# Optimization experiments

Hardware: AMD Instinct MI355X
Metric: run time of the kernel (lower is better)

The kernel has to match this reference:

```python
import jax, jax.numpy as jnp
import numpy as np

B, T, D = 32, 512, 768
DUR_MAX = 8.0


def length_regulate(x, dur):
    # dur[dur < 0] = 0; reps = (dur + 0.5).long()  (floor of dur+0.5 for dur >= 0)
    dur = jnp.maximum(dur, 0.0)
    reps = jnp.floor(dur + 0.5).astype(jnp.int32)          # [B, T]
    cum = jnp.cumsum(reps, axis=1)                          # [B, T] end offsets
    totals = cum[:, -1]                                     # [B] per-sample lengths
    t_out = int(jnp.max(totals))                            # padded output length (data-dependent, eager)
    pos = jnp.arange(t_out, dtype=jnp.int32)                # [Tout]
    # For output slot j, source token index = searchsorted(cum, j, 'right')
    idx = jax.vmap(lambda c: jnp.searchsorted(c, pos, side='right'))(cum)  # [B, Tout]
    idx = jnp.minimum(idx, x.shape[1] - 1)                  # clamp padding region
    out = jnp.take_along_axis(x, idx[..., None], axis=1)    # [B, Tout, D] gather
    mask = pos[None, :] < totals[:, None]                   # [B, Tout]
    return jnp.where(mask[..., None], out, jnp.zeros((), x.dtype))


def setup_inputs() -> dict:
    key = jax.random.key(0)
    k1, k2 = jax.random.split(key)
    x = jax.random.normal(k1, (B, T, D), dtype=jnp.float32)
    dur = jax.random.uniform(k2, (B, T), dtype=jnp.float32, minval=0.0, maxval=DUR_MAX)
    return {"x": x, "dur": dur}


def reference(x, dur):
    return length_regulate(x, dur)
```

## Files before the change

### kernel.cpp

```cpp
#include <hip/hip_runtime.h>

#define BB 32
#define TT 512
#define DD 768
#define ROWS_PER_BLOCK 8
#define VEC_PER_ROW (DD / 4)

__global__ __launch_bounds__(TT) void lr_scan_kernel(
    const float* __restrict__ dur, int* __restrict__ cum) {
    __shared__ int s[TT];
    const int b = blockIdx.x;
    const int t = threadIdx.x;
    float d = dur[b * TT + t];
    d = fmaxf(d, 0.0f);
    s[t] = (int)floorf(d + 0.5f);
    __syncthreads();
    #pragma unroll
    for (int off = 1; off < TT; off <<= 1) {
        int v = (t >= off) ? s[t - off] : 0;
        __syncthreads();
        s[t] += v;
        __syncthreads();
    }
    cum[b * TT + t] = s[t];
}

__global__ __launch_bounds__(VEC_PER_ROW) void lr_gather_kernel(
    const float* __restrict__ x, const int* __restrict__ cum,
    float* __restrict__ out, int t_out) {
    __shared__ int scum[TT];
    const int b = blockIdx.y;
    const int tid = threadIdx.x;

    for (int i = tid; i < TT; i += VEC_PER_ROW) scum[i] = cum[b * TT + i];
    __syncthreads();

    const int total = scum[TT - 1];
    const int row0 = blockIdx.x * ROWS_PER_BLOCK;

    const float4* xb = (const float4*)(x + (size_t)b * TT * DD);
    float4* ob = (float4*)(out + (size_t)b * (size_t)t_out * DD);

    #pragma unroll
    for (int r = 0; r < ROWS_PER_BLOCK; ++r) {
        const int pos = row0 + r;
        if (pos >= t_out) break;
        float4 v;
        if (pos >= total) {
            v = make_float4(0.f, 0.f, 0.f, 0.f);
        } else {
            int lo = 0, hi = TT;
            while (lo < hi) {
                int mid = (lo + hi) >> 1;
                if (scum[mid] <= pos) lo = mid + 1; else hi = mid;
            }
            int idx = lo < (TT - 1) ? lo : (TT - 1);
            v = xb[(size_t)idx * VEC_PER_ROW + tid];
        }
        ob[(size_t)pos * VEC_PER_ROW + tid] = v;
    }
}

extern "C" void kernel_launch(void* const* d_in, const int* in_sizes, int n_in,
                              void* d_out, int out_size, void* d_ws, size_t ws_size,
                              hipStream_t stream) {
    const float* x   = (const float*)d_in[0];
    const float* dur = (const float*)d_in[1];
    float* out = (float*)d_out;
    int* cum = (int*)d_ws;

    const int t_out = out_size / (BB * DD);

    lr_scan_kernel<<<BB, TT, 0, stream>>>(dur, cum);

    dim3 grid((t_out + ROWS_PER_BLOCK - 1) / ROWS_PER_BLOCK, BB);
    lr_gather_kernel<<<grid, VEC_PER_ROW, 0, stream>>>(x, cum, out, t_out);
}
```

Before: 265.3 us.

## Replace per-row binary-search gather with per-token scatter plus tail zeroing

Switches from a gather, where each output row binary-searches the cumulative durations in shared memory, to a scatter, where each source token is loaded once and written to its contiguous output range. A separate kernel zeroes the padding tail beyond each sample's total length. This removes the per-row search and the repeated reads of the same source row, in exchange for an extra kernel launch and per-block work that now varies with each token's duration.

```diff
diff --git a/kernel.cpp b/kernel.cpp
--- a/kernel.cpp
+++ b/kernel.cpp
@@ -3,8 +3,9 @@
 #define BB 32
 #define TT 512
 #define DD 768
-#define ROWS_PER_BLOCK 8
 #define VEC_PER_ROW (DD / 4)
+#define TOK_PER_BLOCK 8
+#define TAIL_ROWS 8
 
 __global__ __launch_bounds__(TT) void lr_scan_kernel(
     const float* __restrict__ dur, int* __restrict__ cum) {
@@ -25,7 +26,7 @@
     cum[b * TT + t] = s[t];
 }
 
-__global__ __launch_bounds__(VEC_PER_ROW) void lr_gather_kernel(
+__global__ __launch_bounds__(VEC_PER_ROW) void lr_scatter_kernel(
     const float* __restrict__ x, const int* __restrict__ cum,
     float* __restrict__ out, int t_out) {
     __shared__ int scum[TT];
@@ -35,29 +36,38 @@
     for (int i = tid; i < TT; i += VEC_PER_ROW) scum[i] = cum[b * TT + i];
     __syncthreads();
 
-    const int total = scum[TT - 1];
-    const int row0 = blockIdx.x * ROWS_PER_BLOCK;
-
+    const int s0 = blockIdx.x * TOK_PER_BLOCK;
     const float4* xb = (const float4*)(x + (size_t)b * TT * DD);
     float4* ob = (float4*)(out + (size_t)b * (size_t)t_out * DD);
 
     #pragma unroll
-    for (int r = 0; r < ROWS_PER_BLOCK; ++r) {
+    for (int k = 0; k < TOK_PER_BLOCK; ++k) {
+        const int t = s0 + k;
+        const int start = (t == 0) ? 0 : scum[t - 1];
+        const int end = scum[t];
+        if (end > start) {
+            const float4 v = xb[(size_t)t * VEC_PER_ROW + tid];
+            for (int p = start; p < end; ++p)
+                ob[(size_t)p * VEC_PER_ROW + tid] = v;
+        }
+    }
+}
+
+__global__ __launch_bounds__(VEC_PER_ROW) void lr_zero_tail_kernel(
+    const int* __restrict__ cum, float* __restrict__ out, int t_out) {
+    const int b = blockIdx.y;
+    const int total = cum[b * TT + (TT - 1)];
+    const int row0 = blockIdx.x * TAIL_ROWS;
+    if (row0 + TAIL_ROWS <= total) return;
+
+    const int tid = threadIdx.x;
+    float4* ob = (float4*)(out + (size_t)b * (size_t)t_out * DD);
+    const float4 z = make_float4(0.f, 0.f, 0.f, 0.f);
+    #pragma unroll
+    for (int r = 0; r < TAIL_ROWS; ++r) {
         const int pos = row0 + r;
-        if (pos >= t_out) break;
-        float4 v;
-        if (pos >= total) {
-            v = make_float4(0.f, 0.f, 0.f, 0.f);
-        } else {
-            int lo = 0, hi = TT;
-            while (lo < hi) {
-                int mid = (lo + hi) >> 1;
-                if (scum[mid] <= pos) lo = mid + 1; else hi = mid;
-            }
-            int idx = lo < (TT - 1) ? lo : (TT - 1);
-            v = xb[(size_t)idx * VEC_PER_ROW + tid];
-        }
-        ob[(size_t)pos * VEC_PER_ROW + tid] = v;
+        if (pos >= total && pos < t_out)
+            ob[(size_t)pos * VEC_PER_ROW + tid] = z;
     }
 }
 
@@ -73,6 +83,9 @@
 
     lr_scan_kernel<<<BB, TT, 0, stream>>>(dur, cum);
 
-    dim3 grid((t_out + ROWS_PER_BLOCK - 1) / ROWS_PER_BLOCK, BB);
-    lr_gather_kernel<<<grid, VEC_PER_ROW, 0, stream>>>(x, cum, out, t_out);
+    dim3 sgrid(TT / TOK_PER_BLOCK, BB);
+    lr_scatter_kernel<<<sgrid, VEC_PER_ROW, 0, stream>>>(x, cum, out, t_out);
+
+    dim3 zgrid((t_out + TAIL_ROWS - 1) / TAIL_ROWS, BB);
+    lr_zero_tail_kernel<<<zgrid, VEC_PER_ROW, 0, stream>>>(cum, out, t_out);
 }
```

Result: no change. 261.7 us (-1.4%).
